# Kernel optimization log

Hardware: AMD Instinct MI355X
Metric: run time of the kernel (lower is better)

## Reference

```python
import math
import jax, jax.numpy as jnp
import numpy as np


def setup_inputs() -> dict:
    key = jax.random.key(0)
    kq, kk, kv, kb, km = jax.random.split(key, 5)
    B, Q, H, C = 2, 2048, 16, 64
    q = jax.random.normal(kq, (B, Q, H, C), jnp.float32)
    k = jax.random.normal(kk, (B, Q, H, C), jnp.float32)
    v = jax.random.normal(kv, (B, Q, H, C), jnp.float32)
    b = jax.random.normal(kb, (B, H, Q, Q), jnp.float32)
    m = jnp.sort(jax.random.randint(km, (B, Q), 0, 4), axis=-1).astype(jnp.int32)
    return {"q": q, "k": k, "v": v, "b": b, "m": m}


def reference(q, k, v, b, m):
    # q,k,v: (B, S, H, C); b: (B, H, S, S); m: (B, S) segment ids (self-attn)
    sm_scale = 1.0 / math.sqrt(q.shape[-1])
    n_q, n_k = q.shape[1], k.shape[1]
    logits = jnp.einsum('bqhc,bkhc->bhqk', q, k).astype(jnp.float32)
    # segment mask: (B, 1, Q, K), True where query/key share a segment id
    seg_mask = (m[:, :, None] == m[:, None, :])[:, None, :, :]
    causal_mask = jnp.tril(jnp.ones((1, 1, n_q, n_k), dtype=bool))
    mask = jnp.logical_and(seg_mask, causal_mask)
    logits = jnp.where(mask, logits, -jnp.inf)
    weights = jax.nn.softmax(logits * sm_scale + b.astype(jnp.float32), axis=-1).astype(q.dtype)
    out = jnp.einsum('bhqk,bkhc->bqhc', weights, v)
    return out.astype(jnp.float32)
```

## Files before the change

kernel.cpp:

```cpp
#include <hip/hip_runtime.h>
#include <hip/hip_bf16.h>
#include <math.h>

#define NB 2
#define SEQ 2048
#define NH 16
#define HD 64
#define QT 64
#define KT 64

typedef short short8 __attribute__((ext_vector_type(8)));
typedef float f32x4 __attribute__((ext_vector_type(4)));
typedef int i32x4 __attribute__((ext_vector_type(4)));
typedef unsigned int u32;
typedef u32 u32x2 __attribute__((ext_vector_type(2)));
typedef u32 u32x4 __attribute__((ext_vector_type(4)));

__device__ __forceinline__ unsigned short f2bf(float f) {
  union { float f; unsigned u; } x; x.f = f;
  unsigned r = x.u + 0x7fffu + ((x.u >> 16) & 1u);
  return (unsigned short)(r >> 16);
}

__device__ __forceinline__ u32 pkbf(float a, float b) {
  u32 r;
  asm("v_cvt_pk_bf16_f32 %0, %1, %2" : "=v"(r) : "v"(a), "v"(b));
  return r;
}

__device__ __forceinline__ void barrier_nodrain() {
  __builtin_amdgcn_sched_barrier(0);
  __builtin_amdgcn_s_barrier();
  __builtin_amdgcn_sched_barrier(0);
}
__device__ __forceinline__ void barrier_nodrain_ldswrites() {
  __builtin_amdgcn_sched_barrier(0);
  asm volatile("s_waitcnt lgkmcnt(0)");
  __builtin_amdgcn_sched_barrier(0);
  __builtin_amdgcn_s_barrier();
  __builtin_amdgcn_sched_barrier(0);
}


__global__ __launch_bounds__(256, 3) void attn_fwd(
    const float* __restrict__ Qg, const float* __restrict__ Kg,
    const float* __restrict__ Vg, const float* __restrict__ Bg,
    const int* __restrict__ Mg, float* __restrict__ Og)
{
  const int h = blockIdx.x, qt = blockIdx.y, b = blockIdx.z;
  const int q0 = qt * QT;
  const int tid = threadIdx.x;
  const int wave = tid >> 6, lane = tid & 63;
  const int l16 = lane & 15, lhi = lane >> 4;

  __shared__ __align__(16) unsigned short Ks[KT][72];
  __shared__ __align__(16) unsigned short Vt[HD][72];
  __shared__ __align__(16) unsigned short Ps[4][16][72];

  const int* mb = Mg + b * SEQ;
  const int mqf = mb[q0];
  const int mql = mb[q0 + QT - 1];
  int lo = 0, hi = q0 + 1;
  while (lo < hi) { int mid = (lo + hi) >> 1; if (mb[mid] < mqf) lo = mid + 1; else hi = mid; }
  const int k_lo = lo;
  lo = 0; hi = q0 + QT;
  while (lo < hi) { int mid = (lo + hi) >> 1; if (mb[mid] <= mql) lo = mid + 1; else hi = mid; }
  const int k_hi = lo;

  const int kt0 = k_lo & ~(KT - 1);
  const int nt = (k_hi - kt0 + KT - 1) / KT;

  const int qr = q0 + wave * 16;

  const float* qp = Qg + (((size_t)b * SEQ + qr + l16) * NH + h) * HD;
  short8 qf[2];
  #pragma unroll
  for (int s = 0; s < 2; ++s) {
    f32x4 a0 = *(const f32x4*)(qp + lhi * 8 + 32 * s);
    f32x4 a1 = *(const f32x4*)(qp + lhi * 8 + 32 * s + 4);
    short8 t;
    #pragma unroll
    for (int i = 0; i < 4; ++i) {
      t[i]     = (short)f2bf(a0[i] * 0.125f);
      t[i + 4] = (short)f2bf(a1[i] * 0.125f);
    }
    qf[s] = t;
  }

  int mq[4];
  #pragma unroll
  for (int j = 0; j < 4; ++j) mq[j] = mb[qr + lhi * 4 + j];

  f32x4 oacc[4];
  float mrun[4], lrun[4];
  #pragma unroll
  for (int g = 0; g < 4; ++g) { f32x4 z = {0.f, 0.f, 0.f, 0.f}; oacc[g] = z; }
  #pragma unroll
  for (int j = 0; j < 4; ++j) { mrun[j] = -1e30f; lrun[j] = 0.f; }

  const int krow = tid >> 2, kc0 = (tid & 3) * 16;
  const int kpr  = ((krow & 3) << 4) | (krow >> 2);
  const int tg   = tid >> 4;
  const int vcv  = (tid & 15) * 4;
  const int vr0  = ((tg & 3) << 4) | (tg >> 2);
  const int vc0  = tg * 4;
  const size_t rstride = (size_t)NH * HD;
  const float* kbase = Kg + (((size_t)b * SEQ + krow) * NH + h) * HD + kc0;
  const float* vbase = Vg + (((size_t)b * SEQ + vr0) * NH + h) * HD + vcv;
  const size_t bbase = (((size_t)b * NH + h) * SEQ) * (size_t)SEQ;

  f32x4 kx0, kx1, kx2, kx3, vx0, vx1, vx2, vx3;
  {
    const float* kp = kbase + (size_t)kt0 * rstride;
    kx0 = *(const f32x4*)(kp);      kx1 = *(const f32x4*)(kp + 4);
    kx2 = *(const f32x4*)(kp + 8);  kx3 = *(const f32x4*)(kp + 12);
    const float* vp = vbase + (size_t)kt0 * rstride;
    vx0 = *(const f32x4*)(vp);
    vx1 = *(const f32x4*)(vp + 4 * rstride);
    vx2 = *(const f32x4*)(vp + 8 * rstride);
    vx3 = *(const f32x4*)(vp + 12 * rstride);
  }

  for (int t = 0; t < nt; ++t) {
    const int k0 = kt0 + t * KT;

    const float* bprow = Bg + bbase + (size_t)(qr + lhi * 4) * SEQ + k0 + 4 * l16;
    f32x4 bv4[4];
    #pragma unroll
    for (int j = 0; j < 4; ++j) bv4[j] = *(const f32x4*)(bprow + (size_t)j * SEQ);
    const i32x4 mk = *(const i32x4*)&mb[k0 + 4 * l16];

    barrier_nodrain();

    {
      u32x4 wa, wb;
      wa[0] = pkbf(kx0[0], kx0[1]); wa[1] = pkbf(kx0[2], kx0[3]);
      wa[2] = pkbf(kx1[0], kx1[1]); wa[3] = pkbf(kx1[2], kx1[3]);
      wb[0] = pkbf(kx2[0], kx2[1]); wb[1] = pkbf(kx2[2], kx2[3]);
      wb[2] = pkbf(kx3[0], kx3[1]); wb[3] = pkbf(kx3[2], kx3[3]);
      *(u32x4*)&Ks[kpr][kc0]     = wa;
      *(u32x4*)&Ks[kpr][kc0 + 8] = wb;
      #pragma unroll
      for (int cc = 0; cc < 4; ++cc) {
        u32x2 wv;
        wv[0] = pkbf(vx0[cc], vx1[cc]);
        wv[1] = pkbf(vx2[cc], vx3[cc]);
        *(u32x2*)&Vt[vcv + cc][vc0] = wv;
      }
    }

    if (t + 1 < nt) {
      const int kn = k0 + KT;
      const float* kp = kbase + (size_t)kn * rstride;
      kx0 = *(const f32x4*)(kp);      kx1 = *(const f32x4*)(kp + 4);
      kx2 = *(const f32x4*)(kp + 8);  kx3 = *(const f32x4*)(kp + 12);
      const float* vp = vbase + (size_t)kn * rstride;
      vx0 = *(const f32x4*)(vp);
      vx1 = *(const f32x4*)(vp + 4 * rstride);
      vx2 = *(const f32x4*)(vp + 8 * rstride);
      vx3 = *(const f32x4*)(vp + 12 * rstride);
    }

    barrier_nodrain_ldswrites();

    f32x4 sacc[4];
    #pragma unroll
    for (int g = 0; g < 4; ++g) { f32x4 z = {0.f, 0.f, 0.f, 0.f}; sacc[g] = z; }
    #pragma unroll
    for (int s = 0; s < 2; ++s) {
      #pragma unroll
      for (int g = 0; g < 4; ++g) {
        short8 kf = *(const short8*)&Ks[l16 + 16 * g][lhi * 8 + 32 * s];
        sacc[g] = __builtin_amdgcn_mfma_f32_16x16x32_bf16(qf[s], kf, sacc[g], 0, 0, 0);
      }
    }

    const int colk = k0 + 4 * l16;
    #pragma unroll
    for (int g = 0; g < 4; ++g) {
      #pragma unroll
      for (int j = 0; j < 4; ++j) {
        const int rowq = qr + lhi * 4 + j;
        const bool ok = (mk[g] == mq[j]) && (colk + g <= rowq);
        sacc[g][j] = ok ? (sacc[g][j] + bv4[j][g]) : -1e30f;
      }
    }

    float resc[4], mnew[4], rsum[4];
    #pragma unroll
    for (int j = 0; j < 4; ++j) {
      float mx = fmaxf(fmaxf(sacc[0][j], sacc[1][j]), fmaxf(sacc[2][j], sacc[3][j]));
      mx = fmaxf(mx, __shfl_xor(mx, 1));
      mx = fmaxf(mx, __shfl_xor(mx, 2));
      mx = fmaxf(mx, __shfl_xor(mx, 4));
      mx = fmaxf(mx, __shfl_xor(mx, 8));
      mnew[j] = fmaxf(mrun[j], mx);
      resc[j] = __expf(mrun[j] - mnew[j]);
      mrun[j] = mnew[j];
      rsum[j] = 0.f;
    }
    #pragma unroll
    for (int g = 0; g < 4; ++g) {
      #pragma unroll
      for (int j = 0; j < 4; ++j) {
        float p = (sacc[g][j] > -9e29f) ? __expf(sacc[g][j] - mnew[j]) : 0.f;
        rsum[j] += p;
        Ps[wave][lhi * 4 + j][l16 + 16 * g] = (unsigned short)pkbf(p, p);
      }
    }
    #pragma unroll
    for (int j = 0; j < 4; ++j) {
      float r = rsum[j];
      r += __shfl_xor(r, 1); r += __shfl_xor(r, 2);
      r += __shfl_xor(r, 4); r += __shfl_xor(r, 8);
      lrun[j] = lrun[j] * resc[j] + r;
    }
    #pragma unroll
    for (int g = 0; g < 4; ++g) {
      #pragma unroll
      for (int j = 0; j < 4; ++j) oacc[g][j] *= resc[j];
    }

    #pragma unroll
    for (int s = 0; s < 2; ++s) {
      short8 pf = *(const short8*)&Ps[wave][l16][lhi * 8 + 32 * s];
      #pragma unroll
      for (int g = 0; g < 4; ++g) {
        short8 vf = *(const short8*)&Vt[l16 + 16 * g][lhi * 8 + 32 * s];
        oacc[g] = __builtin_amdgcn_mfma_f32_16x16x32_bf16(pf, vf, oacc[g], 0, 0, 0);
      }
    }
  }

  #pragma unroll
  for (int j = 0; j < 4; ++j) {
    const float inv = 1.f / lrun[j];
    float* op = Og + (((size_t)b * SEQ + qr + lhi * 4 + j) * NH + h) * HD + l16;
    #pragma unroll
    for (int g = 0; g < 4; ++g) op[16 * g] = oacc[g][j] * inv;
  }
}

extern "C" void kernel_launch(void* const* d_in, const int* in_sizes, int n_in,
                              void* d_out, int out_size, void* d_ws, size_t ws_size,
                              hipStream_t stream) {
  const float* q = (const float*)d_in[0];
  const float* k = (const float*)d_in[1];
  const float* v = (const float*)d_in[2];
  const float* bias = (const float*)d_in[3];
  const int* m = (const int*)d_in[4];
  float* out = (float*)d_out;

  dim3 grid(NH, SEQ / QT, NB);
  dim3 block(256);
  hipLaunchKernelGGL(attn_fwd, grid, block, 0, stream, q, k, v, bias, m, out);
}
```

Baseline: 48.01 us.

## Double-buffer K/V shared tiles and prefetch bias one tile ahead

```diff
diff --git a/kernel.cpp b/kernel.cpp
--- a/kernel.cpp
+++ b/kernel.cpp
@@ -28,12 +28,7 @@
   return r;
 }
 
-__device__ __forceinline__ void barrier_nodrain() {
-  __builtin_amdgcn_sched_barrier(0);
-  __builtin_amdgcn_s_barrier();
-  __builtin_amdgcn_sched_barrier(0);
-}
-__device__ __forceinline__ void barrier_nodrain_ldswrites() {
+__device__ __forceinline__ void barrier_lds() {
   __builtin_amdgcn_sched_barrier(0);
   asm volatile("s_waitcnt lgkmcnt(0)");
   __builtin_amdgcn_sched_barrier(0);
@@ -53,8 +48,8 @@
   const int wave = tid >> 6, lane = tid & 63;
   const int l16 = lane & 15, lhi = lane >> 4;
 
-  __shared__ __align__(16) unsigned short Ks[KT][72];
-  __shared__ __align__(16) unsigned short Vt[HD][72];
+  __shared__ __align__(16) unsigned short Ks[2][KT][72];
+  __shared__ __align__(16) unsigned short Vt[2][HD][72];
   __shared__ __align__(16) unsigned short Ps[4][16][72];
 
   const int* mb = Mg + b * SEQ;
@@ -108,6 +103,7 @@
   const float* kbase = Kg + (((size_t)b * SEQ + krow) * NH + h) * HD + kc0;
   const float* vbase = Vg + (((size_t)b * SEQ + vr0) * NH + h) * HD + vcv;
   const size_t bbase = (((size_t)b * NH + h) * SEQ) * (size_t)SEQ;
+  const float* bprow = Bg + bbase + (size_t)(qr + lhi * 4) * SEQ + 4 * l16;
 
   f32x4 kx0, kx1, kx2, kx3, vx0, vx1, vx2, vx3;
   {
@@ -120,37 +116,70 @@
     vx2 = *(const f32x4*)(vp + 8 * rstride);
     vx3 = *(const f32x4*)(vp + 12 * rstride);
   }
+  f32x4 bv4[4];
+  #pragma unroll
+  for (int j = 0; j < 4; ++j) bv4[j] = *(const f32x4*)(bprow + (size_t)j * SEQ + kt0);
+  i32x4 mk = *(const i32x4*)&mb[kt0 + 4 * l16];
+
+  {
+    u32x4 wa, wb;
+    wa[0] = pkbf(kx0[0], kx0[1]); wa[1] = pkbf(kx0[2], kx0[3]);
+    wa[2] = pkbf(kx1[0], kx1[1]); wa[3] = pkbf(kx1[2], kx1[3]);
+    wb[0] = pkbf(kx2[0], kx2[1]); wb[1] = pkbf(kx2[2], kx2[3]);
+    wb[2] = pkbf(kx3[0], kx3[1]); wb[3] = pkbf(kx3[2], kx3[3]);
+    *(u32x4*)&Ks[0][kpr][kc0]     = wa;
+    *(u32x4*)&Ks[0][kpr][kc0 + 8] = wb;
+    #pragma unroll
+    for (int cc = 0; cc < 4; ++cc) {
+      u32x2 wv;
+      wv[0] = pkbf(vx0[cc], vx1[cc]);
+      wv[1] = pkbf(vx2[cc], vx3[cc]);
+      *(u32x2*)&Vt[0][vcv + cc][vc0] = wv;
+    }
+  }
+  if (nt > 1) {
+    const float* kp = kbase + (size_t)(kt0 + KT) * rstride;
+    kx0 = *(const f32x4*)(kp);      kx1 = *(const f32x4*)(kp + 4);
+    kx2 = *(const f32x4*)(kp + 8);  kx3 = *(const f32x4*)(kp + 12);
+    const float* vp = vbase + (size_t)(kt0 + KT) * rstride;
+    vx0 = *(const f32x4*)(vp);
+    vx1 = *(const f32x4*)(vp + 4 * rstride);
+    vx2 = *(const f32x4*)(vp + 8 * rstride);
+    vx3 = *(const f32x4*)(vp + 12 * rstride);
+  }
+  barrier_lds();
 
   for (int t = 0; t < nt; ++t) {
     const int k0 = kt0 + t * KT;
-
-    const float* bprow = Bg + bbase + (size_t)(qr + lhi * 4) * SEQ + k0 + 4 * l16;
-    f32x4 bv4[4];
-    #pragma unroll
-    for (int j = 0; j < 4; ++j) bv4[j] = *(const f32x4*)(bprow + (size_t)j * SEQ);
-    const i32x4 mk = *(const i32x4*)&mb[k0 + 4 * l16];
-
-    barrier_nodrain();
-
-    {
+    const int cur = t & 1;
+
+    f32x4 bvn[4] = {};
+    i32x4 mkn = {};
+    if (t + 1 < nt) {
+      #pragma unroll
+      for (int j = 0; j < 4; ++j) bvn[j] = *(const f32x4*)(bprow + (size_t)j * SEQ + k0 + KT);
+      mkn = *(const i32x4*)&mb[k0 + KT + 4 * l16];
+    }
+
+    if (t + 1 < nt) {
       u32x4 wa, wb;
       wa[0] = pkbf(kx0[0], kx0[1]); wa[1] = pkbf(kx0[2], kx0[3]);
       wa[2] = pkbf(kx1[0], kx1[1]); wa[3] = pkbf(kx1[2], kx1[3]);
       wb[0] = pkbf(kx2[0], kx2[1]); wb[1] = pkbf(kx2[2], kx2[3]);
       wb[2] = pkbf(kx3[0], kx3[1]); wb[3] = pkbf(kx3[2], kx3[3]);
-      *(u32x4*)&Ks[kpr][kc0]     = wa;
-      *(u32x4*)&Ks[kpr][kc0 + 8] = wb;
+      *(u32x4*)&Ks[cur ^ 1][kpr][kc0]     = wa;
+      *(u32x4*)&Ks[cur ^ 1][kpr][kc0 + 8] = wb;
       #pragma unroll
       for (int cc = 0; cc < 4; ++cc) {
         u32x2 wv;
         wv[0] = pkbf(vx0[cc], vx1[cc]);
         wv[1] = pkbf(vx2[cc], vx3[cc]);
-        *(u32x2*)&Vt[vcv + cc][vc0] = wv;
-      }
-    }
-
-    if (t + 1 < nt) {
-      const int kn = k0 + KT;
+        *(u32x2*)&Vt[cur ^ 1][vcv + cc][vc0] = wv;
+      }
+    }
+
+    if (t + 2 < nt) {
+      const int kn = k0 + 2 * KT;
       const float* kp = kbase + (size_t)kn * rstride;
       kx0 = *(const f32x4*)(kp);      kx1 = *(const f32x4*)(kp + 4);
       kx2 = *(const f32x4*)(kp + 8);  kx3 = *(const f32x4*)(kp + 12);
@@ -161,8 +190,6 @@
       vx3 = *(const f32x4*)(vp + 12 * rstride);
     }
 
-    barrier_nodrain_ldswrites();
-
     f32x4 sacc[4];
     #pragma unroll
     for (int g = 0; g < 4; ++g) { f32x4 z = {0.f, 0.f, 0.f, 0.f}; sacc[g] = z; }
@@ -170,7 +197,7 @@
     for (int s = 0; s < 2; ++s) {
       #pragma unroll
       for (int g = 0; g < 4; ++g) {
-        short8 kf = *(const short8*)&Ks[l16 + 16 * g][lhi * 8 + 32 * s];
+        short8 kf = *(const short8*)&Ks[cur][l16 + 16 * g][lhi * 8 + 32 * s];
         sacc[g] = __builtin_amdgcn_mfma_f32_16x16x32_bf16(qf[s], kf, sacc[g], 0, 0, 0);
       }
     }
@@ -226,10 +253,16 @@
       short8 pf = *(const short8*)&Ps[wave][l16][lhi * 8 + 32 * s];
       #pragma unroll
       for (int g = 0; g < 4; ++g) {
-        short8 vf = *(const short8*)&Vt[l16 + 16 * g][lhi * 8 + 32 * s];
+        short8 vf = *(const short8*)&Vt[cur][l16 + 16 * g][lhi * 8 + 32 * s];
         oacc[g] = __builtin_amdgcn_mfma_f32_16x16x32_bf16(pf, vf, oacc[g], 0, 0, 0);
       }
     }
+
+    barrier_lds();
+
+    #pragma unroll
+    for (int j = 0; j < 4; ++j) bv4[j] = bvn[j];
+    mk = mkn;
   }
 
   #pragma unroll
```

Measured after the change: 54.39 us. 1.13x slower.

## Pre-convert K/V to bf16 in a separate pass and reverse q-tile launch order

Applied to the files above, without the earlier changes.

```diff
diff --git a/kernel.cpp b/kernel.cpp
--- a/kernel.cpp
+++ b/kernel.cpp
@@ -41,13 +41,33 @@
   __builtin_amdgcn_sched_barrier(0);
 }
 
+__global__ __launch_bounds__(256) void cvt_kv(
+    const float* __restrict__ Kg, const float* __restrict__ Vg,
+    u32* __restrict__ Kb, u32* __restrict__ Vb)
+{
+  const size_t i = ((size_t)blockIdx.x * 256 + threadIdx.x) * 8;
+  f32x4 a = *(const f32x4*)(Kg + i);
+  f32x4 c = *(const f32x4*)(Kg + i + 4);
+  u32x4 w;
+  w[0] = pkbf(a[0], a[1]); w[1] = pkbf(a[2], a[3]);
+  w[2] = pkbf(c[0], c[1]); w[3] = pkbf(c[2], c[3]);
+  *(u32x4*)(Kb + i / 2) = w;
+  f32x4 d = *(const f32x4*)(Vg + i);
+  f32x4 e = *(const f32x4*)(Vg + i + 4);
+  u32x4 x;
+  x[0] = pkbf(d[0], d[1]); x[1] = pkbf(d[2], d[3]);
+  x[2] = pkbf(e[0], e[1]); x[3] = pkbf(e[2], e[3]);
+  *(u32x4*)(Vb + i / 2) = x;
+}
+
 
 __global__ __launch_bounds__(256, 3) void attn_fwd(
-    const float* __restrict__ Qg, const float* __restrict__ Kg,
-    const float* __restrict__ Vg, const float* __restrict__ Bg,
+    const float* __restrict__ Qg, const u32* __restrict__ Kb,
+    const u32* __restrict__ Vb, const float* __restrict__ Bg,
     const int* __restrict__ Mg, float* __restrict__ Og)
 {
-  const int h = blockIdx.x, qt = blockIdx.y, b = blockIdx.z;
+  const int h = blockIdx.x, b = blockIdx.z;
+  const int qt = (int)gridDim.y - 1 - (int)blockIdx.y;
   const int q0 = qt * QT;
   const int tid = threadIdx.x;
   const int wave = tid >> 6, lane = tid & 63;
@@ -104,21 +124,20 @@
   const int vcv  = (tid & 15) * 4;
   const int vr0  = ((tg & 3) << 4) | (tg >> 2);
   const int vc0  = tg * 4;
-  const size_t rstride = (size_t)NH * HD;
-  const float* kbase = Kg + (((size_t)b * SEQ + krow) * NH + h) * HD + kc0;
-  const float* vbase = Vg + (((size_t)b * SEQ + vr0) * NH + h) * HD + vcv;
+  const size_t rstride2 = (size_t)NH * (HD / 2);
+  const u32* kb_base = Kb + (((size_t)b * SEQ + krow) * NH + h) * (HD / 2) + (tid & 3) * 8;
+  const u32* vb_base = Vb + (((size_t)b * SEQ + vr0) * NH + h) * (HD / 2) + (tid & 15) * 2;
   const size_t bbase = (((size_t)b * NH + h) * SEQ) * (size_t)SEQ;
 
-  f32x4 kx0, kx1, kx2, kx3, vx0, vx1, vx2, vx3;
+  u32x4 kxa, kxb; u32x2 vl0, vl1, vl2, vl3;
   {
-    const float* kp = kbase + (size_t)kt0 * rstride;
-    kx0 = *(const f32x4*)(kp);      kx1 = *(const f32x4*)(kp + 4);
-    kx2 = *(const f32x4*)(kp + 8);  kx3 = *(const f32x4*)(kp + 12);
-    const float* vp = vbase + (size_t)kt0 * rstride;
-    vx0 = *(const f32x4*)(vp);
-    vx1 = *(const f32x4*)(vp + 4 * rstride);
-    vx2 = *(const f32x4*)(vp + 8 * rstride);
-    vx3 = *(const f32x4*)(vp + 12 * rstride);
+    const u32* kp = kb_base + (size_t)kt0 * rstride2;
+    kxa = *(const u32x4*)(kp); kxb = *(const u32x4*)(kp + 4);
+    const u32* vp = vb_base + (size_t)kt0 * rstride2;
+    vl0 = *(const u32x2*)(vp);
+    vl1 = *(const u32x2*)(vp + 4 * rstride2);
+    vl2 = *(const u32x2*)(vp + 8 * rstride2);
+    vl3 = *(const u32x2*)(vp + 12 * rstride2);
   }
 
   for (int t = 0; t < nt; ++t) {
@@ -133,32 +152,32 @@
     barrier_nodrain();
 
     {
-      u32x4 wa, wb;
-      wa[0] = pkbf(kx0[0], kx0[1]); wa[1] = pkbf(kx0[2], kx0[3]);
-      wa[2] = pkbf(kx1[0], kx1[1]); wa[3] = pkbf(kx1[2], kx1[3]);
-      wb[0] = pkbf(kx2[0], kx2[1]); wb[1] = pkbf(kx2[2], kx2[3]);
-      wb[2] = pkbf(kx3[0], kx3[1]); wb[3] = pkbf(kx3[2], kx3[3]);
-      *(u32x4*)&Ks[kpr][kc0]     = wa;
-      *(u32x4*)&Ks[kpr][kc0 + 8] = wb;
-      #pragma unroll
-      for (int cc = 0; cc < 4; ++cc) {
-        u32x2 wv;
-        wv[0] = pkbf(vx0[cc], vx1[cc]);
-        wv[1] = pkbf(vx2[cc], vx3[cc]);
-        *(u32x2*)&Vt[vcv + cc][vc0] = wv;
-      }
+      *(u32x4*)&Ks[kpr][kc0]     = kxa;
+      *(u32x4*)&Ks[kpr][kc0 + 8] = kxb;
+      u32x2 w0, w1, w2, w3;
+      w0[0] = __builtin_amdgcn_perm(vl1[0], vl0[0], 0x05040100u);
+      w0[1] = __builtin_amdgcn_perm(vl3[0], vl2[0], 0x05040100u);
+      w1[0] = __builtin_amdgcn_perm(vl1[0], vl0[0], 0x07060302u);
+      w1[1] = __builtin_amdgcn_perm(vl3[0], vl2[0], 0x07060302u);
+      w2[0] = __builtin_amdgcn_perm(vl1[1], vl0[1], 0x05040100u);
+      w2[1] = __builtin_amdgcn_perm(vl3[1], vl2[1], 0x05040100u);
+      w3[0] = __builtin_amdgcn_perm(vl1[1], vl0[1], 0x07060302u);
+      w3[1] = __builtin_amdgcn_perm(vl3[1], vl2[1], 0x07060302u);
+      *(u32x2*)&Vt[vcv + 0][vc0] = w0;
+      *(u32x2*)&Vt[vcv + 1][vc0] = w1;
+      *(u32x2*)&Vt[vcv + 2][vc0] = w2;
+      *(u32x2*)&Vt[vcv + 3][vc0] = w3;
     }
 
     if (t + 1 < nt) {
       const int kn = k0 + KT;
-      const float* kp = kbase + (size_t)kn * rstride;
-      kx0 = *(const f32x4*)(kp);      kx1 = *(const f32x4*)(kp + 4);
-      kx2 = *(const f32x4*)(kp + 8);  kx3 = *(const f32x4*)(kp + 12);
-      const float* vp = vbase + (size_t)kn * rstride;
-      vx0 = *(const f32x4*)(vp);
-      vx1 = *(const f32x4*)(vp + 4 * rstride);
-      vx2 = *(const f32x4*)(vp + 8 * rstride);
-      vx3 = *(const f32x4*)(vp + 12 * rstride);
+      const u32* kp = kb_base + (size_t)kn * rstride2;
+      kxa = *(const u32x4*)(kp); kxb = *(const u32x4*)(kp + 4);
+      const u32* vp = vb_base + (size_t)kn * rstride2;
+      vl0 = *(const u32x2*)(vp);
+      vl1 = *(const u32x2*)(vp + 4 * rstride2);
+      vl2 = *(const u32x2*)(vp + 8 * rstride2);
+      vl3 = *(const u32x2*)(vp + 12 * rstride2);
     }
 
     barrier_nodrain_ldswrites();
@@ -251,7 +270,13 @@
   const int* m = (const int*)d_in[4];
   float* out = (float*)d_out;
 
+  u32* Kb = (u32*)d_ws;
+  u32* Vb = Kb + ((size_t)NB * SEQ * NH * HD) / 2;
+
+  const int nElem = NB * SEQ * NH * HD;
+  hipLaunchKernelGGL(cvt_kv, dim3(nElem / (256 * 8)), dim3(256), 0, stream, k, v, Kb, Vb);
+
   dim3 grid(NH, SEQ / QT, NB);
   dim3 block(256);
-  hipLaunchKernelGGL(attn_fwd, grid, block, 0, stream, q, k, v, bias, m, out);
-}
+  hipLaunchKernelGGL(attn_fwd, grid, block, 0, stream, q, Kb, Vb, bias, m, out);
+}
```

Result: slower. 59.90 us (+24.8%).
